# Kernel optimization log

Measured on AMD Instinct MI355X. Metric: run time of the kernel, lower is better.

## Reference

```python
import jax, jax.numpy as jnp
import numpy as np

B, NPG, H, D = 16, 4096, 2, 64            # graphs, nodes/graph, heads, in_channels
N = B * NPG                                # 65536 total nodes
E_PER = 32768                              # edges per graph (avg degree 8)
E = B * E_PER                              # 524288 total edges
K_ORDER = 4
BETA = 0.5
D_OUT = 64


def setup_inputs():
    key = jax.random.key(0)
    k = jax.random.split(key, 10)
    x = jax.random.normal(k[0], (N, D), jnp.float32)
    # intra-graph random edges (block-diagonal adjacency)
    src = jax.random.randint(k[1], (B, E_PER), 0, NPG)
    dst = jax.random.randint(k[2], (B, E_PER), 0, NPG)
    off = (jnp.arange(B) * NPG)[:, None]
    edge_index = jnp.stack([(src + off).reshape(-1), (dst + off).reshape(-1)], axis=0)
    batch = jnp.arange(N) // NPG
    s = 1.0 / np.sqrt(D)
    Wq = jax.random.normal(k[3], (D, D * H), jnp.float32) * s
    bq = jnp.zeros((D * H,), jnp.float32)
    Wk = jax.random.normal(k[4], (D, D * H), jnp.float32) * s
    bk = jnp.zeros((D * H,), jnp.float32)
    Wo = jax.random.normal(k[5], (D * H, D_OUT), jnp.float32) * (1.0 / np.sqrt(D * H))
    bo = jnp.zeros((D_OUT,), jnp.float32)
    return {"x": x, "edge_index": edge_index, "batch": batch,
            "Wq": Wq, "bq": bq, "Wk": Wk, "bk": bk, "Wo": Wo, "bo": bo}


def reference(x, edge_index, batch, Wq, bq, Wk, bk, Wo, bo):
    Nn = x.shape[0]
    q = (x @ Wq + bq).reshape(Nn, H, D)
    k = (x @ Wk + bk).reshape(Nn, H, D)
    qs = q / jnp.linalg.norm(q, axis=2, keepdims=True)
    ks = k / jnp.linalg.norm(k, axis=2, keepdims=True)

    # symmetric-normalized transposed adjacency: adj_t[col_e, row_e] = w_e
    row, col = edge_index[0], edge_index[1]
    w = jnp.ones((row.shape[0],), x.dtype)
    deg = jax.ops.segment_sum(w, col, num_segments=N)
    dinv = jnp.where(deg > 0, deg ** -0.5, 0.0)
    val = dinv[col] * w * dinv[row]

    def gcn(xs):  # xs [N,H,D]; out[i] = sum_{e: col_e==i} val_e * xs[row_e]
        return jax.ops.segment_sum(val[:, None, None] * xs[row], col, num_segments=N)

    # ragged block <-> padded batch conversion (block-sorted batch ids)
    counts = jax.ops.segment_sum(jnp.ones((Nn,), jnp.int32), batch, num_segments=B)
    starts = jnp.concatenate([jnp.zeros((1,), jnp.int32), jnp.cumsum(counts)[:-1]])
    pos = jnp.arange(Nn) - starts[batch]

    def to_batch(v):
        return jnp.zeros((B, NPG) + v.shape[1:], v.dtype).at[batch, pos].set(v)

    def to_block(v):
        return v[batch, pos]

    qs_b, ks_b = to_batch(qs), to_batch(ks)      # [B, NPG, H, D]
    xs = jnp.broadcast_to(x[:, None, :], (Nn, H, D))
    xs_b = to_batch(xs)

    # linear (kernelized) attention; note source adds B (=qs.shape[0]) to the
    # denominator and uses the pre-loop xs_batch for every iteration -- kept faithful.
    kvs = jnp.einsum('blhm,blhd->bhmd', ks_b, xs_b)
    qkvs = jnp.einsum('bnhm,bhmd->bnhd', qs_b, kvs)
    num = qkvs + xs_b.sum(axis=1)[:, None]                       # [B,NPG,H,D]
    den = jnp.einsum('bnhm,bhm->bnh', qs_b, ks_b.sum(axis=1))[..., None] + float(B)
    attn_blk = to_block(num / den)                               # [N,H,D]

    for _ in range(K_ORDER):
        xs = xs + BETA * gcn(xs) + (1.0 - BETA) * attn_blk

    return (xs.reshape(Nn, H * D) @ Wo + bo) / H
```

## Files before the change

kernel.cpp:

```cpp
#include <hip/hip_runtime.h>

#define N_NODES 65536
#define B_G     16
#define NPG_    4096
#define H_H     2
#define D_D     64
#define HD      128
#define E_E     524288
#define D_OUT   64


__global__ void deg_kernel(const int* __restrict__ col, int* __restrict__ degi) {
    int e = blockIdx.x * 256 + threadIdx.x;
    if (e < E_E) atomicAdd(&degi[col[e]], 1);
}

__global__ void scan1(const int* __restrict__ degi, int* __restrict__ ptr,
                      int* __restrict__ bsums, float* __restrict__ dinv) {
    __shared__ int lds[256];
    int t = threadIdx.x;
    int i = blockIdx.x * 256 + t;
    int v = degi[i];
    dinv[i] = (v > 0) ? (1.0f / sqrtf((float)v)) : 0.0f;
    lds[t] = v;
    __syncthreads();
    for (int off = 1; off < 256; off <<= 1) {
        int tmp = (t >= off) ? lds[t - off] : 0;
        __syncthreads();
        lds[t] += tmp;
        __syncthreads();
    }
    ptr[i] = lds[t] - v;
    if (t == 255) bsums[blockIdx.x] = lds[255];
}

__global__ void scan3(int* __restrict__ ptr, const int* __restrict__ bsums) {
    __shared__ int red[256];
    int t = threadIdx.x;
    red[t] = (t < (int)blockIdx.x) ? bsums[t] : 0;
    __syncthreads();
    for (int off = 128; off > 0; off >>= 1) {
        if (t < off) red[t] += red[t + off];
        __syncthreads();
    }
    int i = blockIdx.x * 256 + t;
    ptr[i] += red[0];
    if (i == 0) ptr[N_NODES] = E_E;
}

__global__ void scatter_kernel(const int* __restrict__ row, const int* __restrict__ col,
                               const int* __restrict__ ptr, int* __restrict__ cursor,
                               const float* __restrict__ dinv,
                               int2* __restrict__ ep) {
    int e = blockIdx.x * 256 + threadIdx.x;
    if (e < E_E) {
        int c = col[e], r = row[e];
        int p = ptr[c] + atomicAdd(&cursor[c], 1);
        ep[p] = make_int2(r, __float_as_int(dinv[c] * dinv[r]));
    }
}

__global__ __launch_bounds__(256) void proj_kernel(
    const float* __restrict__ x,
    const float* __restrict__ Wq, const float* __restrict__ bq,
    const float* __restrict__ Wk, const float* __restrict__ bk,
    float* __restrict__ qs, float* __restrict__ ks) {
    __shared__ float4 wt4[16 * 128];
    __shared__ float4 xt4[64 * 17];
    __shared__ float bl[128];
    int t = threadIdx.x;
    int qk = blockIdx.x & 1;
    int nb = (blockIdx.x >> 1) * 64;
    const float* W = qk ? Wk : Wq;
    const float* bias = qk ? bk : bq;
    float* outp = qk ? ks : qs;

    for (int i = t; i < 2048; i += 256) {
        int k4 = i >> 7, c = i & 127;
        wt4[i] = make_float4(W[(4 * k4 + 0) * 128 + c], W[(4 * k4 + 1) * 128 + c],
                             W[(4 * k4 + 2) * 128 + c], W[(4 * k4 + 3) * 128 + c]);
    }
    const float4* xg = (const float4*)(x + (size_t)nb * 64);
    for (int i = t; i < 1024; i += 256) {
        int node = i >> 4, k4 = i & 15;
        xt4[node * 17 + k4] = xg[i];
    }
    if (t < 128) bl[t] = bias[t];
    __syncthreads();

    int cg = t & 15;
    int nd = (t >> 4) & 3;
    int w = t >> 6;
    int n_t = w * 16 + nd * 4;

    float acc[4][8];
#pragma unroll
    for (int i = 0; i < 4; ++i)
#pragma unroll
        for (int j = 0; j < 8; ++j) acc[i][j] = 0.f;

#pragma unroll 2
    for (int k4 = 0; k4 < 16; ++k4) {
        float4 xv0 = xt4[(n_t + 0) * 17 + k4];
        float4 xv1 = xt4[(n_t + 1) * 17 + k4];
        float4 xv2 = xt4[(n_t + 2) * 17 + k4];
        float4 xv3 = xt4[(n_t + 3) * 17 + k4];
#pragma unroll
        for (int j = 0; j < 8; ++j) {
            float4 wv = wt4[k4 * 128 + cg + 16 * j];
            acc[0][j] += wv.x * xv0.x + wv.y * xv0.y + wv.z * xv0.z + wv.w * xv0.w;
            acc[1][j] += wv.x * xv1.x + wv.y * xv1.y + wv.z * xv1.z + wv.w * xv1.w;
            acc[2][j] += wv.x * xv2.x + wv.y * xv2.y + wv.z * xv2.z + wv.w * xv2.w;
            acc[3][j] += wv.x * xv3.x + wv.y * xv3.y + wv.z * xv3.z + wv.w * xv3.w;
        }
    }

    float bcol[8];
#pragma unroll
    for (int j = 0; j < 8; ++j) bcol[j] = bl[cg + 16 * j];

#pragma unroll
    for (int i = 0; i < 4; ++i) {
#pragma unroll
        for (int j = 0; j < 8; ++j) acc[i][j] += bcol[j];
        float s0 = acc[i][0] * acc[i][0] + acc[i][1] * acc[i][1] +
                   acc[i][2] * acc[i][2] + acc[i][3] * acc[i][3];
        float s1 = acc[i][4] * acc[i][4] + acc[i][5] * acc[i][5] +
                   acc[i][6] * acc[i][6] + acc[i][7] * acc[i][7];
#pragma unroll
        for (int off = 8; off > 0; off >>= 1) {
            s0 += __shfl_xor(s0, off);
            s1 += __shfl_xor(s1, off);
        }
        float r0 = rsqrtf(s0), r1 = rsqrtf(s1);
        size_t base = (size_t)(nb + n_t + i) * 128 + cg;
#pragma unroll
        for (int j = 0; j < 4; ++j) outp[base + 16 * j] = acc[i][j] * r0;
#pragma unroll
        for (int j = 4; j < 8; ++j) outp[base + 16 * j] = acc[i][j] * r1;
    }
}

__global__ __launch_bounds__(256) void kvs_part(
    const float* __restrict__ ks, const float* __restrict__ x,
    float* __restrict__ partials, float* __restrict__ ksum, float* __restrict__ xsum) {
    int bid = blockIdx.x;
    int chunk = bid & 31;
    int bh = bid >> 5;
    int b = bh >> 1, h = bh & 1;
    int t = threadIdx.x;
    int mrow = t >> 4, dcol = t & 15;
    int m0 = mrow * 4, d0 = dcol * 4;
    __shared__ float kl[32 * 64];
    __shared__ float xl[32 * 64];
    float acc[4][4] = {{0}};
    float ksacc[4] = {0, 0, 0, 0};
    float xsacc[4] = {0, 0, 0, 0};
    int node0 = b * NPG_ + chunk * 128;
    for (int s = 0; s < 4; ++s) {
        int nb = node0 + s * 32;
        for (int i = t; i < 512; i += 256) {
            int l = i >> 4, q = i & 15;
            ((float4*)kl)[i] = *(const float4*)(ks + (size_t)(nb + l) * 128 + h * 64 + q * 4);
        }
        const float4* xg = (const float4*)(x + (size_t)nb * 64);
        for (int i = t; i < 512; i += 256) ((float4*)xl)[i] = xg[i];
        __syncthreads();
        for (int l = 0; l < 32; ++l) {
            float4 kv = *(float4*)(kl + l * 64 + m0);
            float4 xv = *(float4*)(xl + l * 64 + d0);
            float kk[4] = {kv.x, kv.y, kv.z, kv.w};
            float xx[4] = {xv.x, xv.y, xv.z, xv.w};
#pragma unroll
            for (int i = 0; i < 4; ++i)
#pragma unroll
                for (int j = 0; j < 4; ++j) acc[i][j] += kk[i] * xx[j];
            if (dcol == 0) {
#pragma unroll
                for (int i = 0; i < 4; ++i) ksacc[i] += kk[i];
            }
            if (mrow == 0) {
#pragma unroll
                for (int j = 0; j < 4; ++j) xsacc[j] += xx[j];
            }
        }
        __syncthreads();
    }
    float* pout = partials + (size_t)bid * 4096;
#pragma unroll
    for (int i = 0; i < 4; ++i)
        *(float4*)(pout + (m0 + i) * 64 + d0) =
            make_float4(acc[i][0], acc[i][1], acc[i][2], acc[i][3]);
    if (dcol == 0) {
#pragma unroll
        for (int i = 0; i < 4; ++i) atomicAdd(&ksum[bh * 64 + m0 + i], ksacc[i]);
    }
    if (mrow == 0 && h == 0) {
#pragma unroll
        for (int j = 0; j < 4; ++j) atomicAdd(&xsum[b * 64 + d0 + j], xsacc[j]);
    }
}

__global__ __launch_bounds__(256) void kvs_reduce(
    const float* __restrict__ partials, float* __restrict__ kvs) {
    int i = blockIdx.x * 256 + threadIdx.x;
    int bh = i >> 12, elem = i & 4095;
    const float* p = partials + (size_t)bh * 32 * 4096 + elem;
    float s = 0.f;
#pragma unroll
    for (int c = 0; c < 32; ++c) s += p[c * 4096];
    kvs[i] = s;
}

__global__ __launch_bounds__(256) void attn_kernel(
    const float* __restrict__ qs, const float* __restrict__ kvs,
    const float* __restrict__ ksum, const float* __restrict__ xsum,
    float* __restrict__ attn) {
    __shared__ float ql[128 * 64];
    int bid = blockIdx.x;
    int h = bid & 1;
    int nb = (bid >> 1) * 128;
    int b = nb >> 12;
    int bh = b * 2 + h;
    int t = threadIdx.x;
    int lane = t & 63;
    for (int i = t; i < 128 * 16; i += 256) {
        int r = i >> 4, q4 = i & 15;
        ((float4*)ql)[i] = *(const float4*)(qs + (size_t)(nb + r) * 128 + h * 64 + q4 * 4);
    }
    float kvreg[64];
    const float* kvp = kvs + bh * 4096 + lane;
#pragma unroll
    for (int m = 0; m < 64; ++m) kvreg[m] = kvp[m * 64];
    float ksreg = ksum[bh * 64 + lane];
    float xs_d = xsum[b * 64 + lane];
    __syncthreads();
    int nslot = t >> 6;
    for (int nn = 0; nn < 32; ++nn) {
        int node = nn * 4 + nslot;
        const float* qrow = ql + node * 64;
        float p = qrow[lane] * ksreg;
#pragma unroll
        for (int off = 32; off > 0; off >>= 1) p += __shfl_xor(p, off);
        float den = p + 16.0f;
        float acc = 0.f;
#pragma unroll
        for (int m4 = 0; m4 < 16; ++m4) {
            float4 qv = *(const float4*)(qrow + m4 * 4);
            acc += qv.x * kvreg[4 * m4] + qv.y * kvreg[4 * m4 + 1] +
                   qv.z * kvreg[4 * m4 + 2] + qv.w * kvreg[4 * m4 + 3];
        }
        attn[(size_t)(nb + node) * 128 + h * 64 + lane] = (acc + xs_d) / den;
    }
}

__global__ __launch_bounds__(256) void awo_kernel(
    const float* __restrict__ attn, const float* __restrict__ Wo,
    float* __restrict__ a) {
    __shared__ float wlt[64 * 132];
    int t = threadIdx.x;
    for (int i = t; i < 8192; i += 256) {
        int k = i >> 6, j = i & 63;
        wlt[j * 132 + k] = Wo[i];
    }
    __syncthreads();
    int j = t & 63, ng = t >> 6;
    const float* wj = wlt + j * 132;
    int nbase = blockIdx.x * 64 + ng * 16;
    for (int g = 0; g < 4; ++g) {
        int n0 = nbase + g * 4;
        const float4* xr0 = (const float4*)(attn + (size_t)(n0 + 0) * 128);
        const float4* xr1 = (const float4*)(attn + (size_t)(n0 + 1) * 128);
        const float4* xr2 = (const float4*)(attn + (size_t)(n0 + 2) * 128);
        const float4* xr3 = (const float4*)(attn + (size_t)(n0 + 3) * 128);
        float a0 = 0.f, a1 = 0.f, a2 = 0.f, a3 = 0.f;
#pragma unroll 4
        for (int k4 = 0; k4 < 32; ++k4) {
            float4 w = *(const float4*)(wj + k4 * 4);
            float4 v0 = xr0[k4], v1 = xr1[k4], v2 = xr2[k4], v3 = xr3[k4];
            a0 += w.x * v0.x + w.y * v0.y + w.z * v0.z + w.w * v0.w;
            a1 += w.x * v1.x + w.y * v1.y + w.z * v1.z + w.w * v1.w;
            a2 += w.x * v2.x + w.y * v2.y + w.z * v2.z + w.w * v2.w;
            a3 += w.x * v3.x + w.y * v3.y + w.z * v3.z + w.w * v3.w;
        }
        a[(size_t)(n0 + 0) * 64 + j] = a0;
        a[(size_t)(n0 + 1) * 64 + j] = a1;
        a[(size_t)(n0 + 2) * 64 + j] = a2;
        a[(size_t)(n0 + 3) * 64 + j] = a3;
    }
}

__global__ __launch_bounds__(256) void y0_kernel(
    const float* __restrict__ x, const float* __restrict__ Wo,
    float* __restrict__ y0) {
    __shared__ float wl[64 * 68];
    int t = threadIdx.x;
    for (int i = t; i < 4096; i += 256) {
        int k = i >> 6, j = i & 63;
        wl[j * 68 + k] = Wo[k * 64 + j] + Wo[(k + 64) * 64 + j];
    }
    __syncthreads();
    int j = t & 63, ng = t >> 6;
    const float* wj = wl + j * 68;
    int nbase = blockIdx.x * 64 + ng * 16;
    for (int g = 0; g < 4; ++g) {
        int n0 = nbase + g * 4;
        const float4* xr0 = (const float4*)(x + (size_t)(n0 + 0) * 64);
        const float4* xr1 = (const float4*)(x + (size_t)(n0 + 1) * 64);
        const float4* xr2 = (const float4*)(x + (size_t)(n0 + 2) * 64);
        const float4* xr3 = (const float4*)(x + (size_t)(n0 + 3) * 64);
        float a0 = 0.f, a1 = 0.f, a2 = 0.f, a3 = 0.f;
#pragma unroll 4
        for (int k4 = 0; k4 < 16; ++k4) {
            float4 w = *(const float4*)(wj + k4 * 4);
            float4 v0 = xr0[k4], v1 = xr1[k4], v2 = xr2[k4], v3 = xr3[k4];
            a0 += w.x * v0.x + w.y * v0.y + w.z * v0.z + w.w * v0.w;
            a1 += w.x * v1.x + w.y * v1.y + w.z * v1.z + w.w * v1.w;
            a2 += w.x * v2.x + w.y * v2.y + w.z * v2.z + w.w * v2.w;
            a3 += w.x * v3.x + w.y * v3.y + w.z * v3.z + w.w * v3.w;
        }
        y0[(size_t)(n0 + 0) * 64 + j] = a0;
        y0[(size_t)(n0 + 1) * 64 + j] = a1;
        y0[(size_t)(n0 + 2) * 64 + j] = a2;
        y0[(size_t)(n0 + 3) * 64 + j] = a3;
    }
}

template <int LAST>
__global__ __launch_bounds__(256) void gcn64_kernel(
    const float* __restrict__ yin, const float* __restrict__ a,
    const int* __restrict__ ptr, const int2* __restrict__ ep,
    float* __restrict__ yout, const float* __restrict__ bo) {
    int bid = blockIdx.x;
    int lbid = (bid & 7) * (N_NODES / 16 / 8) + (bid >> 3);
    int t = threadIdx.x;
    int n = lbid * 16 + (t >> 4);
    int lg = t & 15;
    int c4 = lg * 4;
    int e0 = ptr[n], e1 = ptr[n + 1];
    int cnt = e1 - e0;
    float4 acc = make_float4(0.f, 0.f, 0.f, 0.f);

    {
        int2 q[8];
#pragma unroll
        for (int i = 0; i < 8; ++i) {
            int ee = e0 + i;
            if (ee > e1 - 1) ee = e1 - 1;
            if (ee < 0) ee = 0;
            q[i] = ep[ee];
        }
#pragma unroll
        for (int i = 0; i < 8; ++i) {
            if (i < cnt) {
                float v = __int_as_float(q[i].y);
                float4 xv = *(const float4*)(yin + (size_t)q[i].x * 64 + c4);
                acc.x += v * xv.x; acc.y += v * xv.y;
                acc.z += v * xv.z; acc.w += v * xv.w;
            }
        }
    }
    if (cnt > 8) {
        int2 q[8];
#pragma unroll
        for (int i = 0; i < 8; ++i) {
            int ee = e0 + 8 + i;
            if (ee > e1 - 1) ee = e1 - 1;
            q[i] = ep[ee];
        }
#pragma unroll
        for (int i = 0; i < 8; ++i) {
            if (8 + i < cnt) {
                float v = __int_as_float(q[i].y);
                float4 xv = *(const float4*)(yin + (size_t)q[i].x * 64 + c4);
                acc.x += v * xv.x; acc.y += v * xv.y;
                acc.z += v * xv.z; acc.w += v * xv.w;
            }
        }
        for (int e = e0 + 16; e < e1; ++e) {
            int2 qq = ep[e];
            float v = __int_as_float(qq.y);
            float4 xv = *(const float4*)(yin + (size_t)qq.x * 64 + c4);
            acc.x += v * xv.x; acc.y += v * xv.y;
            acc.z += v * xv.z; acc.w += v * xv.w;
        }
    }

    size_t idx = (size_t)n * 64 + c4;
    float4 self = *(const float4*)(yin + idx);
    float4 at = *(const float4*)(a + idx);
    float4 o;
    o.x = self.x + 0.5f * acc.x + 0.5f * at.x;
    o.y = self.y + 0.5f * acc.y + 0.5f * at.y;
    o.z = self.z + 0.5f * acc.z + 0.5f * at.z;
    o.w = self.w + 0.5f * acc.w + 0.5f * at.w;
    if (LAST) {
        float4 bv = *(const float4*)(bo + c4);
        o.x = (o.x + bv.x) * 0.5f;
        o.y = (o.y + bv.y) * 0.5f;
        o.z = (o.z + bv.z) * 0.5f;
        o.w = (o.w + bv.w) * 0.5f;
    }
    *(float4*)(yout + idx) = o;
}


extern "C" void kernel_launch(void* const* d_in, const int* in_sizes, int n_in,
                              void* d_out, int out_size, void* d_ws, size_t ws_size,
                              hipStream_t stream) {
    const float* x  = (const float*)d_in[0];
    const int* ei   = (const int*)d_in[1];
    const float* Wq = (const float*)d_in[3];
    const float* bq = (const float*)d_in[4];
    const float* Wk = (const float*)d_in[5];
    const float* bk = (const float*)d_in[6];
    const float* Wo = (const float*)d_in[7];
    const float* bo = (const float*)d_in[8];
    float* out = (float*)d_out;

    const int* row = ei;
    const int* col = ei + E_E;

    float* bufA = (float*)d_ws;
    float* bufB = bufA + (size_t)N_NODES * HD;
    float* bufC = bufB + (size_t)N_NODES * HD;
    int2*  ep   = (int2*)(bufC + (size_t)N_NODES * HD);
    float* kvs  = (float*)(ep + E_E);
    float* ksum = kvs + 131072;
    float* xsum = ksum + 2048;
    float* dinv = xsum + 1024;
    int* degi   = (int*)(dinv + N_NODES);
    int* cursor = degi + N_NODES;
    int* ptr    = cursor + N_NODES;
    int* bsums  = ptr + N_NODES + 1;

    float* a_  = bufA;
    float* yA  = bufA + (size_t)N_NODES * 64;
    float* yB  = bufB;

    hipMemsetAsync(degi, 0, (size_t)N_NODES * 2 * 4, stream);
    hipMemsetAsync(ksum, 0, (size_t)(2048 + 1024) * 4, stream);

    deg_kernel<<<E_E / 256, 256, 0, stream>>>(col, degi);
    scan1<<<N_NODES / 256, 256, 0, stream>>>(degi, ptr, bsums, dinv);
    scan3<<<N_NODES / 256, 256, 0, stream>>>(ptr, bsums);
    scatter_kernel<<<E_E / 256, 256, 0, stream>>>(row, col, ptr, cursor, dinv, ep);

    proj_kernel<<<2048, 256, 0, stream>>>(x, Wq, bq, Wk, bk, bufA, bufB);

    kvs_part<<<1024, 256, 0, stream>>>(bufB, x, bufC, ksum, xsum);
    kvs_reduce<<<512, 256, 0, stream>>>(bufC, kvs);
    attn_kernel<<<1024, 256, 0, stream>>>(bufA, kvs, ksum, xsum, bufC);

    awo_kernel<<<1024, 256, 0, stream>>>(bufC, Wo, a_);
    y0_kernel<<<1024, 256, 0, stream>>>(x, Wo, yA);

    gcn64_kernel<0><<<N_NODES / 16, 256, 0, stream>>>(yA, a_, ptr, ep, yB, bo);
    gcn64_kernel<0><<<N_NODES / 16, 256, 0, stream>>>(yB, a_, ptr, ep, yA, bo);
    gcn64_kernel<0><<<N_NODES / 16, 256, 0, stream>>>(yA, a_, ptr, ep, yB, bo);
    gcn64_kernel<1><<<N_NODES / 16, 256, 0, stream>>>(yB, a_, ptr, ep, out, bo);
}
```

Measured before the change: 419.1 us.

## Register-tile awo and y0 projections with LDS-staged inputs and XOR-swizzled k

Rewrites the two small dense projection kernels (attn@Wo and x@Wo_sum) to stage both the weight tile and the 64-node input tile in shared memory as float4. Each thread now computes a 4x4 output micro-tile, with an XOR swizzle on the k index to spread LDS bank access. Before, each thread read its input rows straight from global memory per output column, so the same rows were loaded by many threads. The change cuts that redundant global traffic and adds reuse in registers, at the cost of more LDS and higher register pressure.

```diff
diff --git a/kernel.cpp b/kernel.cpp
--- a/kernel.cpp
+++ b/kernel.cpp
@@ -257,73 +257,96 @@
 __global__ __launch_bounds__(256) void awo_kernel(
     const float* __restrict__ attn, const float* __restrict__ Wo,
     float* __restrict__ a) {
-    __shared__ float wlt[64 * 132];
-    int t = threadIdx.x;
-    for (int i = t; i < 8192; i += 256) {
-        int k = i >> 6, j = i & 63;
-        wlt[j * 132 + k] = Wo[i];
-    }
-    __syncthreads();
-    int j = t & 63, ng = t >> 6;
-    const float* wj = wlt + j * 132;
-    int nbase = blockIdx.x * 64 + ng * 16;
-    for (int g = 0; g < 4; ++g) {
-        int n0 = nbase + g * 4;
-        const float4* xr0 = (const float4*)(attn + (size_t)(n0 + 0) * 128);
-        const float4* xr1 = (const float4*)(attn + (size_t)(n0 + 1) * 128);
-        const float4* xr2 = (const float4*)(attn + (size_t)(n0 + 2) * 128);
-        const float4* xr3 = (const float4*)(attn + (size_t)(n0 + 3) * 128);
-        float a0 = 0.f, a1 = 0.f, a2 = 0.f, a3 = 0.f;
+    __shared__ float4 wt4[32 * 64];
+    __shared__ float4 xt4[64 * 32];
+    int t = threadIdx.x;
+    int nb = blockIdx.x * 64;
+
+    for (int i = t; i < 2048; i += 256) {
+        int k4 = i >> 6, c = i & 63;
+        wt4[i] = make_float4(Wo[(4 * k4 + 0) * 64 + c], Wo[(4 * k4 + 1) * 64 + c],
+                             Wo[(4 * k4 + 2) * 64 + c], Wo[(4 * k4 + 3) * 64 + c]);
+    }
+    const float4* ag = (const float4*)(attn + (size_t)nb * 128);
+    for (int i = t; i < 2048; i += 256) xt4[i] = ag[i];
+    __syncthreads();
+
+    int cg = t & 15;
+    int ns = t >> 4;
+    int s = ns & 3;
+    int n_t = ns * 4;
+
+    float acc[4][4] = {{0.f}};
 #pragma unroll 4
-        for (int k4 = 0; k4 < 32; ++k4) {
-            float4 w = *(const float4*)(wj + k4 * 4);
-            float4 v0 = xr0[k4], v1 = xr1[k4], v2 = xr2[k4], v3 = xr3[k4];
-            a0 += w.x * v0.x + w.y * v0.y + w.z * v0.z + w.w * v0.w;
-            a1 += w.x * v1.x + w.y * v1.y + w.z * v1.z + w.w * v1.w;
-            a2 += w.x * v2.x + w.y * v2.y + w.z * v2.z + w.w * v2.w;
-            a3 += w.x * v3.x + w.y * v3.y + w.z * v3.z + w.w * v3.w;
-        }
-        a[(size_t)(n0 + 0) * 64 + j] = a0;
-        a[(size_t)(n0 + 1) * 64 + j] = a1;
-        a[(size_t)(n0 + 2) * 64 + j] = a2;
-        a[(size_t)(n0 + 3) * 64 + j] = a3;
-    }
+    for (int k4 = 0; k4 < 32; ++k4) {
+        int kk = k4 ^ s;
+        float4 xv0 = xt4[(n_t + 0) * 32 + kk];
+        float4 xv1 = xt4[(n_t + 1) * 32 + kk];
+        float4 xv2 = xt4[(n_t + 2) * 32 + kk];
+        float4 xv3 = xt4[(n_t + 3) * 32 + kk];
+#pragma unroll
+        for (int j = 0; j < 4; ++j) {
+            float4 wv = wt4[kk * 64 + cg + 16 * j];
+            acc[0][j] += wv.x * xv0.x + wv.y * xv0.y + wv.z * xv0.z + wv.w * xv0.w;
+            acc[1][j] += wv.x * xv1.x + wv.y * xv1.y + wv.z * xv1.z + wv.w * xv1.w;
+            acc[2][j] += wv.x * xv2.x + wv.y * xv2.y + wv.z * xv2.z + wv.w * xv2.w;
+            acc[3][j] += wv.x * xv3.x + wv.y * xv3.y + wv.z * xv3.z + wv.w * xv3.w;
+        }
+    }
+#pragma unroll
+    for (int i = 0; i < 4; ++i)
+#pragma unroll
+        for (int j = 0; j < 4; ++j)
+            a[(size_t)(nb + n_t + i) * 64 + cg + 16 * j] = acc[i][j];
 }
 
 __global__ __launch_bounds__(256) void y0_kernel(
     const float* __restrict__ x, const float* __restrict__ Wo,
     float* __restrict__ y0) {
-    __shared__ float wl[64 * 68];
-    int t = threadIdx.x;
-    for (int i = t; i < 4096; i += 256) {
-        int k = i >> 6, j = i & 63;
-        wl[j * 68 + k] = Wo[k * 64 + j] + Wo[(k + 64) * 64 + j];
-    }
-    __syncthreads();
-    int j = t & 63, ng = t >> 6;
-    const float* wj = wl + j * 68;
-    int nbase = blockIdx.x * 64 + ng * 16;
-    for (int g = 0; g < 4; ++g) {
-        int n0 = nbase + g * 4;
-        const float4* xr0 = (const float4*)(x + (size_t)(n0 + 0) * 64);
-        const float4* xr1 = (const float4*)(x + (size_t)(n0 + 1) * 64);
-        const float4* xr2 = (const float4*)(x + (size_t)(n0 + 2) * 64);
-        const float4* xr3 = (const float4*)(x + (size_t)(n0 + 3) * 64);
-        float a0 = 0.f, a1 = 0.f, a2 = 0.f, a3 = 0.f;
+    __shared__ float4 wt4[16 * 64];
+    __shared__ float4 xt4[64 * 16];
+    int t = threadIdx.x;
+    int nb = blockIdx.x * 64;
+
+    for (int i = t; i < 1024; i += 256) {
+        int k4 = i >> 6, c = i & 63;
+        wt4[i] = make_float4(
+            Wo[(4 * k4 + 0) * 64 + c] + Wo[(4 * k4 + 64) * 64 + c],
+            Wo[(4 * k4 + 1) * 64 + c] + Wo[(4 * k4 + 65) * 64 + c],
+            Wo[(4 * k4 + 2) * 64 + c] + Wo[(4 * k4 + 66) * 64 + c],
+            Wo[(4 * k4 + 3) * 64 + c] + Wo[(4 * k4 + 67) * 64 + c]);
+    }
+    const float4* xg = (const float4*)(x + (size_t)nb * 64);
+    for (int i = t; i < 1024; i += 256) xt4[i] = xg[i];
+    __syncthreads();
+
+    int cg = t & 15;
+    int ns = t >> 4;
+    int s = ns & 3;
+    int n_t = ns * 4;
+
+    float acc[4][4] = {{0.f}};
 #pragma unroll 4
-        for (int k4 = 0; k4 < 16; ++k4) {
-            float4 w = *(const float4*)(wj + k4 * 4);
-            float4 v0 = xr0[k4], v1 = xr1[k4], v2 = xr2[k4], v3 = xr3[k4];
-            a0 += w.x * v0.x + w.y * v0.y + w.z * v0.z + w.w * v0.w;
-            a1 += w.x * v1.x + w.y * v1.y + w.z * v1.z + w.w * v1.w;
-            a2 += w.x * v2.x + w.y * v2.y + w.z * v2.z + w.w * v2.w;
-            a3 += w.x * v3.x + w.y * v3.y + w.z * v3.z + w.w * v3.w;
-        }
-        y0[(size_t)(n0 + 0) * 64 + j] = a0;
-        y0[(size_t)(n0 + 1) * 64 + j] = a1;
-        y0[(size_t)(n0 + 2) * 64 + j] = a2;
-        y0[(size_t)(n0 + 3) * 64 + j] = a3;
-    }
+    for (int k4 = 0; k4 < 16; ++k4) {
+        int kk = k4 ^ s;
+        float4 xv0 = xt4[(n_t + 0) * 16 + kk];
+        float4 xv1 = xt4[(n_t + 1) * 16 + kk];
+        float4 xv2 = xt4[(n_t + 2) * 16 + kk];
+        float4 xv3 = xt4[(n_t + 3) * 16 + kk];
+#pragma unroll
+        for (int j = 0; j < 4; ++j) {
+            float4 wv = wt4[kk * 64 + cg + 16 * j];
+            acc[0][j] += wv.x * xv0.x + wv.y * xv0.y + wv.z * xv0.z + wv.w * xv0.w;
+            acc[1][j] += wv.x * xv1.x + wv.y * xv1.y + wv.z * xv1.z + wv.w * xv1.w;
+            acc[2][j] += wv.x * xv2.x + wv.y * xv2.y + wv.z * xv2.z + wv.w * xv2.w;
+            acc[3][j] += wv.x * xv3.x + wv.y * xv3.y + wv.z * xv3.z + wv.w * xv3.w;
+        }
+    }
+#pragma unroll
+    for (int i = 0; i < 4; ++i)
+#pragma unroll
+        for (int j = 0; j < 4; ++j)
+            y0[(size_t)(nb + n_t + i) * 64 + cg + 16 * j] = acc[i][j];
 }
 
 template <int LAST>
```

After: 357.6 us. 14.7% less time.
